# Performance work log

Measured on AMD Instinct MI355X. Metric: run time of the kernel, lower is better.

The kernel has to match this reference:

```python
import jax, jax.numpy as jnp
import numpy as np

B, T, MODEL_DIM = 4, 4096, 2048
NUM_HEADS = 16
HEAD_K_DIM = 128
PE_DIM = HEAD_K_DIM // 2  # 64
PHI_RANK = 16
D_CONV = 4
THETA = 500000.0
TEMP_MAX = 1.0
L2_EPS = 1e-6


def setup_inputs() -> dict:
    key = jax.random.key(0)
    ks = jax.random.split(key, 6)
    D = NUM_HEADS * PE_DIM  # 1024 conv channels
    return {
        "q": jax.random.normal(ks[0], (B, T, NUM_HEADS, HEAD_K_DIM), dtype=jnp.float32),
        "k": jax.random.normal(ks[1], (B, T, NUM_HEADS, HEAD_K_DIM), dtype=jnp.float32),
        "hidden_states": jax.random.normal(ks[2], (B, T, MODEL_DIM), dtype=jnp.float32),
        # low-rank phi projection: Linear(model_dim -> rank), Linear(rank -> H*pe_dim), no bias
        "W1": jax.random.normal(ks[3], (MODEL_DIM, PHI_RANK), dtype=jnp.float32) / np.sqrt(MODEL_DIM),
        "W2": jax.random.normal(ks[4], (PHI_RANK, D), dtype=jnp.float32) / np.sqrt(PHI_RANK),
        # depthwise causal short-conv weight in WIO layout: (kernel_w, 1, channels)
        "conv_w": jax.random.normal(ks[5], (D_CONV, 1, D), dtype=jnp.float32) / np.sqrt(D_CONV),
    }


def _rope_temperature():
    # temp_max / theta ** (arange(0, head_k_dim, 2) / head_k_dim) -> [pe_dim]
    exps = jnp.arange(0, HEAD_K_DIM, 2, dtype=jnp.float32) / HEAD_K_DIM
    return TEMP_MAX / (THETA ** exps)


def reference(q, k, hidden_states, W1, W2, conv_w):
    b, t, _ = hidden_states.shape
    # l2-normalize per-head hidden states
    h = hidden_states.reshape(b, t, NUM_HEADS, MODEL_DIM // NUM_HEADS)
    h = h * jax.lax.rsqrt(jnp.sum(h * h, axis=-1, keepdims=True) + L2_EPS)
    x = h.reshape(b, t, MODEL_DIM)
    # low-rank phi projection: [b, t, H*pe_dim]
    phi = (x @ W1) @ W2
    # causal depthwise short convolution over time (kernel 4, no bias, no act)
    D = phi.shape[-1]
    phi = jax.lax.conv_general_dilated(
        phi, conv_w,
        window_strides=(1,),
        padding=[(D_CONV - 1, 0)],
        dimension_numbers=("NWC", "WIO", "NWC"),
        feature_group_count=D,
    )
    phi = phi.reshape(b, t, NUM_HEADS, PE_DIM)
    # cumulative phase
    phi_tilde = jnp.cumsum(phi, axis=1)  # [b, t, H, pe]
    temperature = _rope_temperature()  # [pe]
    # rotate q and k with selective angles
    qk = jnp.concatenate([q, k], axis=2).astype(jnp.float32)  # [b, t, 2H, hd]
    qk0, qk1 = qk[..., :PE_DIM], qk[..., PE_DIM:]
    angle = temperature * jnp.concatenate([phi_tilde, phi_tilde], axis=2)  # [b, t, 2H, pe]
    cos, sin = jnp.cos(angle), jnp.sin(angle)
    rot = jnp.concatenate([qk0 * cos - qk1 * sin, qk0 * sin + qk1 * cos], axis=-1)
    rot = rot.astype(q.dtype)
    return rot[:, :, :NUM_HEADS], rot[:, :, NUM_HEADS:]
```

## Files before the change

kernel.cpp:

```cpp
#include <hip/hip_runtime.h>

#define BB 4
#define TT 4096
#define NH 16
#define HK 128
#define PE 64
#define DD 1024
#define RK 16
#define MD 2048
#define NC 64
#define CS 64

__global__ __launch_bounds__(256) void k1_u(const float* __restrict__ hidden,
                                            const float* __restrict__ W1,
                                            float* __restrict__ u) {
  __shared__ float hs[4 * 64 * 64];
  __shared__ float w1t[4 * 64 * RK];

  const int tid  = threadIdx.x;
  const int lane = tid & 63;
  const int kg   = tid >> 6;
  const int tok0 = blockIdx.x * 64;

  float* hw = hs  + kg * (64 * 64);
  float* ww = w1t + kg * (64 * RK);
  const int kbase = kg * 512;

  float4 hreg[16];
  float4 wreg[4];

#pragma unroll
  for (int it = 0; it < 16; ++it) {
    int idx = it * 64 + lane;
    int tr = idx >> 4, q = idx & 15;
    hreg[it] = *(const float4*)(hidden + (size_t)(tok0 + tr) * MD + kbase + q * 4);
  }
#pragma unroll
  for (int it = 0; it < 4; ++it) {
    int idx = it * 64 + lane;
    wreg[it] = *(const float4*)(W1 + (size_t)kbase * RK + idx * 4);
  }

  float ssH = 0.f;
  float accH[RK];
  float accF[RK];
#pragma unroll
  for (int r = 0; r < RK; ++r) { accH[r] = 0.f; accF[r] = 0.f; }

  for (int dc = 0; dc < 8; ++dc) {
#pragma unroll
    for (int it = 0; it < 16; ++it) {
      int idx = it * 64 + lane;
      int tr = idx >> 4, q = idx & 15;
      int base = tr * 64;
      int sw = tr & 31;
      hw[base + ((q * 4 + 0) ^ sw)] = hreg[it].x;
      hw[base + ((q * 4 + 1) ^ sw)] = hreg[it].y;
      hw[base + ((q * 4 + 2) ^ sw)] = hreg[it].z;
      hw[base + ((q * 4 + 3) ^ sw)] = hreg[it].w;
    }
#pragma unroll
    for (int it = 0; it < 4; ++it) {
      int idx = it * 64 + lane;
      *(float4*)(ww + idx * 4) = wreg[it];
    }

    if (dc < 7) {
      const int kb = kbase + (dc + 1) * 64;
#pragma unroll
      for (int it = 0; it < 16; ++it) {
        int idx = it * 64 + lane;
        int tr = idx >> 4, q = idx & 15;
        hreg[it] = *(const float4*)(hidden + (size_t)(tok0 + tr) * MD + kb + q * 4);
      }
#pragma unroll
      for (int it = 0; it < 4; ++it) {
        int idx = it * 64 + lane;
        wreg[it] = *(const float4*)(W1 + (size_t)kb * RK + idx * 4);
      }
    }

    const int sw = lane & 31;
    const float* hrow = hw + lane * 64;
#pragma unroll 8
    for (int d = 0; d < 64; ++d) {
      float e = hrow[d ^ sw];
      ssH += e * e;
      const float4* wr = (const float4*)(ww + d * RK);
      float4 w0 = wr[0], w1v = wr[1], w2v = wr[2], w3v = wr[3];
      accH[0]  += e * w0.x;  accH[1]  += e * w0.y;  accH[2]  += e * w0.z;  accH[3]  += e * w0.w;
      accH[4]  += e * w1v.x; accH[5]  += e * w1v.y; accH[6]  += e * w1v.z; accH[7]  += e * w1v.w;
      accH[8]  += e * w2v.x; accH[9]  += e * w2v.y; accH[10] += e * w2v.z; accH[11] += e * w2v.w;
      accH[12] += e * w3v.x; accH[13] += e * w3v.y; accH[14] += e * w3v.z; accH[15] += e * w3v.w;
    }

    if (dc & 1) {
      float inv = rsqrtf(ssH + 1e-6f);
#pragma unroll
      for (int r = 0; r < RK; ++r) { accF[r] += accH[r] * inv; accH[r] = 0.f; }
      ssH = 0.f;
    }
  }

  __syncthreads();
  float* red = hs;
  {
    float* rp = red + (kg * 64 + lane) * 17;
#pragma unroll
    for (int r = 0; r < RK; ++r) rp[r] = accF[r];
  }
  __syncthreads();
  {
    int tok = tid >> 2, rq = tid & 3;
    float o0 = 0.f, o1 = 0.f, o2 = 0.f, o3 = 0.f;
#pragma unroll
    for (int g = 0; g < 4; ++g) {
      const float* rp = red + (g * 64 + tok) * 17;
      o0 += rp[rq * 4 + 0];
      o1 += rp[rq * 4 + 1];
      o2 += rp[rq * 4 + 2];
      o3 += rp[rq * 4 + 3];
    }
    float4 o = make_float4(o0, o1, o2, o3);
    *(float4*)(u + (size_t)(tok0 + tok) * RK + rq * 4) = o;
  }
}

__device__ __forceinline__ float phi_raw(const float* __restrict__ ub, int t,
                                         const float* __restrict__ w2r) {
  if (t < 0) return 0.f;
  const float4* up = (const float4*)(ub + (size_t)t * RK);
  float4 u0 = up[0], u1 = up[1], u2 = up[2], u3 = up[3];
  return u0.x * w2r[0]  + u0.y * w2r[1]  + u0.z * w2r[2]  + u0.w * w2r[3]
       + u1.x * w2r[4]  + u1.y * w2r[5]  + u1.z * w2r[6]  + u1.w * w2r[7]
       + u2.x * w2r[8]  + u2.y * w2r[9]  + u2.z * w2r[10] + u2.w * w2r[11]
       + u3.x * w2r[12] + u3.y * w2r[13] + u3.z * w2r[14] + u3.w * w2r[15];
}

__global__ __launch_bounds__(256) void k2_csum(const float* __restrict__ u,
                                               const float* __restrict__ W2,
                                               const float* __restrict__ cw,
                                               float* __restrict__ csum) {
  int tid = threadIdx.x;
  int blk = blockIdx.x;
  int dblk = blk & 3;
  int bc = blk >> 2;
  int chunk = bc & (NC - 1);
  int b = bc >> 6;
  int d = dblk * 256 + tid;

  float w2r[RK];
#pragma unroll
  for (int r = 0; r < RK; ++r) w2r[r] = W2[r * DD + d];
  float c0 = cw[0 * DD + d], c1 = cw[1 * DD + d];
  float c2 = cw[2 * DD + d], c3 = cw[3 * DD + d];

  const float* ub = u + (size_t)b * TT * RK;
  int t0 = chunk * CS;
  float w0 = phi_raw(ub, t0 - 3, w2r);
  float w1 = phi_raw(ub, t0 - 2, w2r);
  float w2v = phi_raw(ub, t0 - 1, w2r);

  float acc = 0.f;
  for (int i = 0; i < CS; ++i) {
    float pr = phi_raw(ub, t0 + i, w2r);
    float cv = c0 * w0 + c1 * w1 + c2 * w2v + c3 * pr;
    w0 = w1; w1 = w2v; w2v = pr;
    acc += cv;
  }
  csum[(size_t)bc * DD + d] = acc;
}

__global__ __launch_bounds__(256) void k3_scan(const float* __restrict__ csum,
                                               float* __restrict__ cpre) {
  int idx = blockIdx.x * 256 + threadIdx.x;
  int b = idx >> 10;
  int d = idx & (DD - 1);
  float run = 0.f;
  for (int c = 0; c < NC; ++c) {
    size_t o = (size_t)(b * NC + c) * DD + d;
    float v = csum[o];
    cpre[o] = run;
    run += v;
  }
}

__global__ __launch_bounds__(64) void k4_apply(const float* __restrict__ u,
                                               const float* __restrict__ W2,
                                               const float* __restrict__ cw,
                                               const float* __restrict__ cpre,
                                               const float* __restrict__ q,
                                               const float* __restrict__ kk,
                                               float* __restrict__ oq,
                                               float* __restrict__ ok) {
  int p = threadIdx.x;
  int blk = blockIdx.x;
  int h = blk & 15;
  int bc = blk >> 4;
  int chunk = bc & (NC - 1);
  int b = bc >> 6;
  int d = h * PE + p;

  float w2r[RK];
#pragma unroll
  for (int r = 0; r < RK; ++r) w2r[r] = W2[r * DD + d];
  float c0 = cw[0 * DD + d], c1 = cw[1 * DD + d];
  float c2 = cw[2 * DD + d], c3 = cw[3 * DD + d];

  float temp = exp2f(-(float)p * (18.93156856932417f / 64.f));

  const float* ub = u + (size_t)b * TT * RK;
  float s = cpre[(size_t)bc * DD + d];

  int t0 = chunk * CS;
  float w0 = phi_raw(ub, t0 - 3, w2r);
  float w1 = phi_raw(ub, t0 - 2, w2r);
  float w2v = phi_raw(ub, t0 - 1, w2r);

  int qbase = ((b * TT + t0) * NH + h) * HK + p;
  for (int i = 0; i < CS; ++i) {
    float pr = phi_raw(ub, t0 + i, w2r);
    float cv = c0 * w0 + c1 * w1 + c2 * w2v + c3 * pr;
    w0 = w1; w1 = w2v; w2v = pr;
    s += cv;

    float ang = temp * s;
    float sn, cn;
    __sincosf(ang, &sn, &cn);

    int off = qbase + i * (NH * HK);
    float q0 = q[off], q1 = q[off + PE];
    float k0 = kk[off], k1 = kk[off + PE];
    oq[off]      = q0 * cn - q1 * sn;
    oq[off + PE] = q0 * sn + q1 * cn;
    ok[off]      = k0 * cn - k1 * sn;
    ok[off + PE] = k0 * sn + k1 * cn;
  }
}

extern "C" void kernel_launch(void* const* d_in, const int* in_sizes, int n_in,
                              void* d_out, int out_size, void* d_ws, size_t ws_size,
                              hipStream_t stream) {
  const float* q      = (const float*)d_in[0];
  const float* k      = (const float*)d_in[1];
  const float* hidden = (const float*)d_in[2];
  const float* W1     = (const float*)d_in[3];
  const float* W2     = (const float*)d_in[4];
  const float* convw  = (const float*)d_in[5];
  float* out = (float*)d_out;

  float* u    = (float*)d_ws;
  float* csum = u + (size_t)BB * TT * RK;
  float* cpre = csum + (size_t)BB * NC * DD;

  k1_u<<<(BB * TT) / 64, 256, 0, stream>>>(hidden, W1, u);
  k2_csum<<<BB * NC * 4, 256, 0, stream>>>(u, W2, convw, csum);
  k3_scan<<<(BB * DD) / 256, 256, 0, stream>>>(csum, cpre);
  k4_apply<<<BB * NC * NH, 64, 0, stream>>>(u, W2, convw, cpre, q, k, out,
                                            out + (size_t)BB * TT * NH * HK);
}
```

Measured before the change: 587.1 us.

## Stage u chunks in LDS, regroup apply blocks, prefetch q/k, unroll scan

Both the chunk-sum and apply kernels now stage the 67 token rows of u needed by a chunk into shared memory once per block. Before, every thread re-read them from global memory with a t<0 branch on each step. The apply kernel now runs 256-thread blocks covering four heads, so the staged u is shared across heads, and it prefetches the next token's q/k values one iteration ahead. The scan kernel is unrolled by 8 so several independent loads are in flight at once. The cost is an extra barrier, more LDS use and more registers.

```diff
diff --git a/kernel.cpp b/kernel.cpp
--- a/kernel.cpp
+++ b/kernel.cpp
@@ -126,10 +126,9 @@
   }
 }
 
-__device__ __forceinline__ float phi_raw(const float* __restrict__ ub, int t,
+__device__ __forceinline__ float phi_lds(const float* __restrict__ us, int j,
                                          const float* __restrict__ w2r) {
-  if (t < 0) return 0.f;
-  const float4* up = (const float4*)(ub + (size_t)t * RK);
+  const float4* up = (const float4*)(us + j * RK);
   float4 u0 = up[0], u1 = up[1], u2 = up[2], u3 = up[3];
   return u0.x * w2r[0]  + u0.y * w2r[1]  + u0.z * w2r[2]  + u0.w * w2r[3]
        + u1.x * w2r[4]  + u1.y * w2r[5]  + u1.z * w2r[6]  + u1.w * w2r[7]
@@ -137,10 +136,24 @@
        + u3.x * w2r[12] + u3.y * w2r[13] + u3.z * w2r[14] + u3.w * w2r[15];
 }
 
+__device__ __forceinline__ void stage_u(const float* __restrict__ ub, int t0,
+                                        float* __restrict__ us, int tid) {
+  for (int idx = tid; idx < 67 * 4; idx += 256) {
+    int j = idx >> 2, rq = idx & 3;
+    int t = t0 - 3 + j;
+    float4 v = make_float4(0.f, 0.f, 0.f, 0.f);
+    if (t >= 0) v = *(const float4*)(ub + (size_t)t * RK + rq * 4);
+    *(float4*)(us + j * RK + rq * 4) = v;
+  }
+  __syncthreads();
+}
+
 __global__ __launch_bounds__(256) void k2_csum(const float* __restrict__ u,
                                                const float* __restrict__ W2,
                                                const float* __restrict__ cw,
                                                float* __restrict__ csum) {
+  __shared__ float us[67 * RK];
+
   int tid = threadIdx.x;
   int blk = blockIdx.x;
   int dblk = blk & 3;
@@ -148,6 +161,9 @@
   int chunk = bc & (NC - 1);
   int b = bc >> 6;
   int d = dblk * 256 + tid;
+  int t0 = chunk * CS;
+
+  stage_u(u + (size_t)b * TT * RK, t0, us, tid);
 
   float w2r[RK];
 #pragma unroll
@@ -155,15 +171,14 @@
   float c0 = cw[0 * DD + d], c1 = cw[1 * DD + d];
   float c2 = cw[2 * DD + d], c3 = cw[3 * DD + d];
 
-  const float* ub = u + (size_t)b * TT * RK;
-  int t0 = chunk * CS;
-  float w0 = phi_raw(ub, t0 - 3, w2r);
-  float w1 = phi_raw(ub, t0 - 2, w2r);
-  float w2v = phi_raw(ub, t0 - 1, w2r);
+  float w0 = phi_lds(us, 0, w2r);
+  float w1 = phi_lds(us, 1, w2r);
+  float w2v = phi_lds(us, 2, w2r);
 
   float acc = 0.f;
+#pragma unroll 4
   for (int i = 0; i < CS; ++i) {
-    float pr = phi_raw(ub, t0 + i, w2r);
+    float pr = phi_lds(us, i + 3, w2r);
     float cv = c0 * w0 + c1 * w1 + c2 * w2v + c3 * pr;
     w0 = w1; w1 = w2v; w2v = pr;
     acc += cv;
@@ -176,30 +191,49 @@
   int idx = blockIdx.x * 256 + threadIdx.x;
   int b = idx >> 10;
   int d = idx & (DD - 1);
+  size_t o = (size_t)b * NC * DD + d;
   float run = 0.f;
-  for (int c = 0; c < NC; ++c) {
-    size_t o = (size_t)(b * NC + c) * DD + d;
-    float v = csum[o];
-    cpre[o] = run;
-    run += v;
-  }
-}
-
-__global__ __launch_bounds__(64) void k4_apply(const float* __restrict__ u,
-                                               const float* __restrict__ W2,
-                                               const float* __restrict__ cw,
-                                               const float* __restrict__ cpre,
-                                               const float* __restrict__ q,
-                                               const float* __restrict__ kk,
-                                               float* __restrict__ oq,
-                                               float* __restrict__ ok) {
-  int p = threadIdx.x;
+  for (int c = 0; c < NC; c += 8) {
+    float v0 = csum[o + 0 * DD], v1 = csum[o + 1 * DD];
+    float v2 = csum[o + 2 * DD], v3 = csum[o + 3 * DD];
+    float v4 = csum[o + 4 * DD], v5 = csum[o + 5 * DD];
+    float v6 = csum[o + 6 * DD], v7 = csum[o + 7 * DD];
+    cpre[o + 0 * DD] = run; run += v0;
+    cpre[o + 1 * DD] = run; run += v1;
+    cpre[o + 2 * DD] = run; run += v2;
+    cpre[o + 3 * DD] = run; run += v3;
+    cpre[o + 4 * DD] = run; run += v4;
+    cpre[o + 5 * DD] = run; run += v5;
+    cpre[o + 6 * DD] = run; run += v6;
+    cpre[o + 7 * DD] = run; run += v7;
+    o += 8 * (size_t)DD;
+  }
+}
+
+__global__ __launch_bounds__(256) void k4_apply(const float* __restrict__ u,
+                                                const float* __restrict__ W2,
+                                                const float* __restrict__ cw,
+                                                const float* __restrict__ cpre,
+                                                const float* __restrict__ q,
+                                                const float* __restrict__ kk,
+                                                float* __restrict__ oq,
+                                                float* __restrict__ ok) {
+  __shared__ float us[67 * RK];
+
+  int tid = threadIdx.x;
+  int lane = tid & 63;
+  int wave = tid >> 6;
   int blk = blockIdx.x;
-  int h = blk & 15;
-  int bc = blk >> 4;
+  int hq = blk & 3;
+  int bc = blk >> 2;
   int chunk = bc & (NC - 1);
   int b = bc >> 6;
+  int h = hq * 4 + wave;
+  int p = lane;
   int d = h * PE + p;
+  int t0 = chunk * CS;
+
+  stage_u(u + (size_t)b * TT * RK, t0, us, tid);
 
   float w2r[RK];
 #pragma unroll
@@ -209,17 +243,25 @@
 
   float temp = exp2f(-(float)p * (18.93156856932417f / 64.f));
 
-  const float* ub = u + (size_t)b * TT * RK;
   float s = cpre[(size_t)bc * DD + d];
 
-  int t0 = chunk * CS;
-  float w0 = phi_raw(ub, t0 - 3, w2r);
-  float w1 = phi_raw(ub, t0 - 2, w2r);
-  float w2v = phi_raw(ub, t0 - 1, w2r);
-
-  int qbase = ((b * TT + t0) * NH + h) * HK + p;
+  float w0 = phi_lds(us, 0, w2r);
+  float w1 = phi_lds(us, 1, w2r);
+  float w2v = phi_lds(us, 2, w2r);
+
+  int off = ((b * TT + t0) * NH + h) * HK + p;
+  float q0 = q[off], q1 = q[off + PE];
+  float k0 = kk[off], k1 = kk[off + PE];
+
   for (int i = 0; i < CS; ++i) {
-    float pr = phi_raw(ub, t0 + i, w2r);
+    float q0n = 0.f, q1n = 0.f, k0n = 0.f, k1n = 0.f;
+    int offn = off + NH * HK;
+    if (i + 1 < CS) {
+      q0n = q[offn]; q1n = q[offn + PE];
+      k0n = kk[offn]; k1n = kk[offn + PE];
+    }
+
+    float pr = phi_lds(us, i + 3, w2r);
     float cv = c0 * w0 + c1 * w1 + c2 * w2v + c3 * pr;
     w0 = w1; w1 = w2v; w2v = pr;
     s += cv;
@@ -228,13 +270,13 @@
     float sn, cn;
     __sincosf(ang, &sn, &cn);
 
-    int off = qbase + i * (NH * HK);
-    float q0 = q[off], q1 = q[off + PE];
-    float k0 = kk[off], k1 = kk[off + PE];
     oq[off]      = q0 * cn - q1 * sn;
     oq[off + PE] = q0 * sn + q1 * cn;
     ok[off]      = k0 * cn - k1 * sn;
     ok[off + PE] = k0 * sn + k1 * cn;
+
+    q0 = q0n; q1 = q1n; k0 = k0n; k1 = k1n;
+    off = offn;
   }
 }
 
@@ -256,6 +298,6 @@
   k1_u<<<(BB * TT) / 64, 256, 0, stream>>>(hidden, W1, u);
   k2_csum<<<BB * NC * 4, 256, 0, stream>>>(u, W2, convw, csum);
   k3_scan<<<(BB * DD) / 256, 256, 0, stream>>>(csum, cpre);
-  k4_apply<<<BB * NC * NH, 64, 0, stream>>>(u, W2, convw, cpre, q, k, out,
+  k4_apply<<<BB * NC * 4, 256, 0, stream>>>(u, W2, convw, cpre, q, k, out,
                                             out + (size_t)BB * TT * NH * HK);
 }
```

Result: no change. 579.4 us (-1.3%).
